# Kernel optimization log

Measured on AMD Instinct MI355X. Metric: run time of the kernel, lower is better.

Reference implementation:

```python
import jax, jax.numpy as jnp
import numpy as np

B, H, W = 32, 64, 1024
D, L, HEADS, E, TOPK, HID, V = 256, 6, 8, 8, 2, 1024, 8000


def _conv(x, w, b, s):
    y = jax.lax.conv_general_dilated(x, w, (s, s), [(1, 1), (1, 1)],
                                     dimension_numbers=('NCHW', 'OIHW', 'NCHW'))
    return y + b[None, :, None, None]


def _gelu(v):
    return jax.nn.gelu(v, approximate=False)


def _ln(x, g, b):
    m = x.mean(-1, keepdims=True)
    v = jnp.mean((x - m) ** 2, -1, keepdims=True)
    return (x - m) * jax.lax.rsqrt(v + 1e-5) * g + b


def _pos(t, c):
    pos = jnp.arange(t, dtype=jnp.float32)[:, None]
    div = jnp.exp(jnp.arange(0, c, 2, dtype=jnp.float32) * (-np.log(10000.0) / c))
    pe = jnp.zeros((t, c), jnp.float32)
    pe = pe.at[:, 0::2].set(jnp.sin(pos * div)).at[:, 1::2].set(jnp.cos(pos * div))
    return pe[None]


def _mha(y, w, b, ow, ob):
    Bq, T, Dm = y.shape
    hd = Dm // HEADS
    qkv = y @ w.T + b
    q, k, v = jnp.split(qkv, 3, axis=-1)
    sh = lambda z: z.reshape(Bq, T, HEADS, hd).transpose(0, 2, 1, 3)
    q, k, v = sh(q), sh(k), sh(v)
    att = jax.nn.softmax(jnp.einsum('bhqd,bhkd->bhqk', q, k) / np.sqrt(hd).astype(np.float32), axis=-1)
    o = jnp.einsum('bhqk,bhkd->bhqd', att, v).transpose(0, 2, 1, 3).reshape(Bq, T, Dm)
    return o @ ow.T + ob


def _moe(y, rw, rb, w1, b1, w2, b2):
    logits = y @ rw.T + rb                      # [B,T,E]
    tlog, tidx = jax.lax.top_k(logits, TOPK)
    gates = jax.nn.softmax(tlog, axis=-1)        # [B,T,K]
    # combine weights per expert: sum_k gate_k * 1[idx_k == e]
    comb = jnp.sum(gates[..., None] * jax.nn.one_hot(tidx, E, dtype=y.dtype), axis=-2)  # [B,T,E]
    h = _gelu(jnp.einsum('btd,ehd->beth', y, w1) + b1[None, :, None, :])
    eo = jnp.einsum('beth,edh->betd', h, w2) + b2[None, :, None, :]
    out = jnp.einsum('bte,betd->btd', comb, eo)
    imp = jax.nn.softmax(logits, axis=-1).mean(axis=(0, 1))
    aux = jnp.mean((imp - 1.0 / E) ** 2)
    return out, aux


def _forward(x, cw1, cb1, cw2, cb2, cw3, cb3, cw4, cb4,
             ln1_g, ln1_b, qkv_w, qkv_b, out_w, out_b,
             ln2_g, ln2_b, router_w, router_b, e_w1, e_b1, e_w2, e_b2,
             normf_g, normf_b, head_w, head_b):
    f = _gelu(_conv(x, cw1, cb1, 2))
    f = _gelu(_conv(f, cw2, cb2, 2))
    f = _gelu(_conv(f, cw3, cb3, 2))
    f = _gelu(_conv(f, cw4, cb4, 1))          # [B,D,H/8,W/8]
    tok = f.mean(axis=2).transpose(0, 2, 1)    # [B,T,D], T=W/8
    h = tok + _pos(tok.shape[1], tok.shape[2])
    aux_total = jnp.asarray(0.0, h.dtype)
    for l in range(L):
        y = _mha(_ln(h, ln1_g[l], ln1_b[l]), qkv_w[l], qkv_b[l], out_w[l], out_b[l])
        h = h + y
        y, aux = _moe(_ln(h, ln2_g[l], ln2_b[l]), router_w[l], router_b[l],
                      e_w1[l], e_b1[l], e_w2[l], e_b2[l])
        h = h + y
        aux_total = aux_total + aux
    h = _ln(h, normf_g, normf_b)
    logits = h @ head_w.T + head_b
    return logits, aux_total / L


def setup_inputs() -> dict:
    key = jax.random.key(0)
    ks = iter(jax.random.split(key, 40))
    nrm = lambda shape: jax.random.normal(next(ks), shape, jnp.float32) * 0.02
    d = {}
    d['x'] = jax.random.normal(next(ks), (B, 1, H, W), jnp.float32)
    d['cw1'] = nrm((D // 4, 1, 3, 3));      d['cb1'] = jnp.zeros((D // 4,), jnp.float32)
    d['cw2'] = nrm((D // 2, D // 4, 3, 3)); d['cb2'] = jnp.zeros((D // 2,), jnp.float32)
    d['cw3'] = nrm((D, D // 2, 3, 3));      d['cb3'] = jnp.zeros((D,), jnp.float32)
    d['cw4'] = nrm((D, D, 3, 3));           d['cb4'] = jnp.zeros((D,), jnp.float32)
    d['ln1_g'] = jnp.ones((L, D), jnp.float32); d['ln1_b'] = jnp.zeros((L, D), jnp.float32)
    d['qkv_w'] = nrm((L, 3 * D, D));        d['qkv_b'] = jnp.zeros((L, 3 * D), jnp.float32)
    d['out_w'] = nrm((L, D, D));            d['out_b'] = jnp.zeros((L, D), jnp.float32)
    d['ln2_g'] = jnp.ones((L, D), jnp.float32); d['ln2_b'] = jnp.zeros((L, D), jnp.float32)
    d['router_w'] = nrm((L, E, D));         d['router_b'] = jnp.zeros((L, E), jnp.float32)
    d['e_w1'] = nrm((L, E, HID, D));        d['e_b1'] = jnp.zeros((L, E, HID), jnp.float32)
    d['e_w2'] = nrm((L, E, D, HID));        d['e_b2'] = jnp.zeros((L, E, D), jnp.float32)
    d['normf_g'] = jnp.ones((D,), jnp.float32); d['normf_b'] = jnp.zeros((D,), jnp.float32)
    d['head_w'] = nrm((V, D));              d['head_b'] = jnp.zeros((V,), jnp.float32)
    return d


def reference(x, cw1, cb1, cw2, cb2, cw3, cb3, cw4, cb4,
              ln1_g, ln1_b, qkv_w, qkv_b, out_w, out_b,
              ln2_g, ln2_b, router_w, router_b, e_w1, e_b1, e_w2, e_b2,
              normf_g, normf_b, head_w, head_b):
    return _forward(x, cw1, cb1, cw2, cb2, cw3, cb3, cw4, cb4,
                    ln1_g, ln1_b, qkv_w, qkv_b, out_w, out_b,
                    ln2_g, ln2_b, router_w, router_b, e_w1, e_b1, e_w2, e_b2,
                    normf_g, normf_b, head_w, head_b)
```

## Files before the change

kernel.cpp:

```cpp
#include <hip/hip_runtime.h>
#include <math.h>


typedef __bf16 bf16x8 __attribute__((ext_vector_type(8)));
typedef float f32x4 __attribute__((ext_vector_type(4)));

__device__ __forceinline__ float gelu_f(float x) {
  return 0.5f * x * (1.0f + erff(x * 0.70710678118654752440f));
}

__global__ __launch_bounds__(256) void conv1_kernel(const float* __restrict__ x,
    const float* __restrict__ w, const float* __restrict__ bias, float* __restrict__ out) {
  int o = blockIdx.x * 256 + threadIdx.x;
  int co = o & 63, wo = (o >> 6) & 511, ho = (o >> 15) & 31, b = o >> 20;
  float acc = bias[co];
  const float* xp = x + (size_t)b * 65536;
  const float* wp = w + co * 9;
  #pragma unroll
  for (int kh = 0; kh < 3; kh++) {
    int hi = ho * 2 - 1 + kh;
    if ((unsigned)hi < 64u) {
      const float* row = xp + hi * 1024;
      #pragma unroll
      for (int kw = 0; kw < 3; kw++) {
        int wi = wo * 2 - 1 + kw;
        if ((unsigned)wi < 1024u) acc += row[wi] * wp[kh * 3 + kw];
      }
    }
  }
  out[o] = gelu_f(acc);
}

__global__ __launch_bounds__(256) void tr_cw_bf16_kernel(const float* __restrict__ w,
    __bf16* __restrict__ hi, __bf16* __restrict__ lo, int CI, int CO) {
  int i = blockIdx.x * 256 + threadIdx.x;
  if (i >= 9 * CI * CO) return;
  int ci = i % CI; int r = i / CI; int co = r % CO; int tap = r / CO;
  float x = w[(co * CI + ci) * 9 + tap];
  __bf16 h = (__bf16)x;
  __bf16 l = (__bf16)(x - (float)h);
  hi[i] = h; lo[i] = l;
}

template <int CI, int HI, int WI, int CO, int HO, int WO, int S>
__global__ __launch_bounds__(256) void convmfma_kernel(
    const float* __restrict__ in, const __bf16* __restrict__ wthi,
    const __bf16* __restrict__ wtlo, const float* __restrict__ bias,
    float* __restrict__ out) {
  __shared__ __bf16 Ah[128 * 40], Al[128 * 40], Bh[128 * 40], Bl[128 * 40];
  int tid = threadIdx.x;
  int lane = tid & 63, wid = tid >> 6;
  int wr = (wid >> 1) << 6, wc = (wid & 1) << 6;
  int lr = lane & 15;
  int lk = (lane >> 4) << 3;
  int tileN = blockIdx.x * 128, tileM = blockIdx.y * 128;
  int tr = tid >> 1;
  int tk = (tid & 1) << 4;
  int m = tileM + tr;
  int wo = m % WO, ho = (m / WO) % HO, b = m / (WO * HO);
  f32x4 acc[4][4];
  #pragma unroll
  for (int i = 0; i < 4; i++)
    #pragma unroll
    for (int j = 0; j < 4; j++) acc[i][j] = (f32x4){0.f, 0.f, 0.f, 0.f};

  for (int tap = 0; tap < 9; tap++) {
    int kh = tap / 3, kw = tap - kh * 3;
    int hi_ = ho * S - 1 + kh, wi_ = wo * S - 1 + kw;
    bool ok = ((unsigned)hi_ < (unsigned)HI) && ((unsigned)wi_ < (unsigned)WI);
    const float* ip = in + ((size_t)(b * HI + hi_) * WI + wi_) * CI + tk;
    const __bf16* wph = wthi + ((size_t)tap * CO + tileN + tr) * CI + tk;
    const __bf16* wpl = wtlo + ((size_t)tap * CO + tileN + tr) * CI + tk;
    for (int c0 = 0; c0 < CI; c0 += 32) {
      float v[16];
      #pragma unroll
      for (int q = 0; q < 4; q++) {
        float4 t4 = ok ? *(const float4*)(ip + c0 + q * 4) : (float4){0.f, 0.f, 0.f, 0.f};
        v[q * 4 + 0] = t4.x; v[q * 4 + 1] = t4.y; v[q * 4 + 2] = t4.z; v[q * 4 + 3] = t4.w;
      }
      bf16x8 hv0, hv1, lv0, lv1;
      #pragma unroll
      for (int j = 0; j < 8; j++) {
        __bf16 h0 = (__bf16)v[j];       hv0[j] = h0;
        lv0[j] = (__bf16)(v[j] - (float)h0);
        __bf16 h1 = (__bf16)v[8 + j];   hv1[j] = h1;
        lv1[j] = (__bf16)(v[8 + j] - (float)h1);
      }
      *(bf16x8*)&Ah[tr * 40 + tk] = hv0;
      *(bf16x8*)&Ah[tr * 40 + tk + 8] = hv1;
      *(bf16x8*)&Al[tr * 40 + tk] = lv0;
      *(bf16x8*)&Al[tr * 40 + tk + 8] = lv1;
      *(uint4*)&Bh[tr * 40 + tk] = *(const uint4*)(wph + c0);
      *(uint4*)&Bh[tr * 40 + tk + 8] = *(const uint4*)(wph + c0 + 8);
      *(uint4*)&Bl[tr * 40 + tk] = *(const uint4*)(wpl + c0);
      *(uint4*)&Bl[tr * 40 + tk + 8] = *(const uint4*)(wpl + c0 + 8);
      __syncthreads();
      bf16x8 ah[4], al[4];
      #pragma unroll
      for (int mt = 0; mt < 4; mt++) {
        int r = wr + mt * 16 + lr;
        ah[mt] = *(const bf16x8*)&Ah[r * 40 + lk];
        al[mt] = *(const bf16x8*)&Al[r * 40 + lk];
      }
      #pragma unroll
      for (int nt = 0; nt < 4; nt++) {
        int cc = wc + nt * 16 + lr;
        bf16x8 bh = *(const bf16x8*)&Bh[cc * 40 + lk];
        bf16x8 bl = *(const bf16x8*)&Bl[cc * 40 + lk];
        #pragma unroll
        for (int mt = 0; mt < 4; mt++) {
          acc[mt][nt] = __builtin_amdgcn_mfma_f32_16x16x32_bf16(ah[mt], bh, acc[mt][nt], 0, 0, 0);
          acc[mt][nt] = __builtin_amdgcn_mfma_f32_16x16x32_bf16(al[mt], bh, acc[mt][nt], 0, 0, 0);
          acc[mt][nt] = __builtin_amdgcn_mfma_f32_16x16x32_bf16(ah[mt], bl, acc[mt][nt], 0, 0, 0);
        }
      }
      __syncthreads();
    }
  }
  int drow = (lane >> 4) << 2;
  #pragma unroll
  for (int mt = 0; mt < 4; mt++) {
    #pragma unroll
    for (int nt = 0; nt < 4; nt++) {
      int orow = tileM + wr + mt * 16 + drow;
      int ocol = tileN + wc + nt * 16 + lr;
      float bv = bias[ocol];
      #pragma unroll
      for (int r = 0; r < 4; r++)
        out[(size_t)(orow + r) * CO + ocol] = gelu_f(acc[mt][nt][r] + bv);
    }
  }
}

__global__ __launch_bounds__(256) void gemm8_kernel(const float* __restrict__ A,
    const float* __restrict__ W, const float* __restrict__ bias, float* __restrict__ C,
    int N, int K, int addTo, int m0, int m1) {
  __shared__ float As[16][132];
  __shared__ float Ws[16][132];
  int tid = threadIdx.x;
  int tileN = blockIdx.x * 128, tileM = m0 + blockIdx.y * 128;
  int tx = tid & 15, ty = tid >> 4;
  int ar = tid >> 1, ak = (tid & 1) << 3;
  float acc[8][8];
  #pragma unroll
  for (int i = 0; i < 8; i++)
    #pragma unroll
    for (int j = 0; j < 8; j++) acc[i][j] = 0.0f;
  int arow = tileM + ar; if (arow > m1 - 1) arow = m1 - 1;
  int wrow = tileN + ar; if (wrow > N - 1) wrow = N - 1;
  const float* Ap = A + (size_t)arow * K + ak;
  const float* Wp = W + (size_t)wrow * K + ak;
  for (int k0 = 0; k0 < K; k0 += 16) {
    float4 a0 = *(const float4*)(Ap + k0);
    float4 a1 = *(const float4*)(Ap + k0 + 4);
    float4 w0 = *(const float4*)(Wp + k0);
    float4 w1 = *(const float4*)(Wp + k0 + 4);
    As[ak + 0][ar] = a0.x; As[ak + 1][ar] = a0.y; As[ak + 2][ar] = a0.z; As[ak + 3][ar] = a0.w;
    As[ak + 4][ar] = a1.x; As[ak + 5][ar] = a1.y; As[ak + 6][ar] = a1.z; As[ak + 7][ar] = a1.w;
    Ws[ak + 0][ar] = w0.x; Ws[ak + 1][ar] = w0.y; Ws[ak + 2][ar] = w0.z; Ws[ak + 3][ar] = w0.w;
    Ws[ak + 4][ar] = w1.x; Ws[ak + 5][ar] = w1.y; Ws[ak + 6][ar] = w1.z; Ws[ak + 7][ar] = w1.w;
    __syncthreads();
    #pragma unroll
    for (int kk = 0; kk < 16; kk++) {
      float4 av0 = *(const float4*)&As[kk][ty << 2];
      float4 av1 = *(const float4*)&As[kk][(ty << 2) + 64];
      float4 wv0 = *(const float4*)&Ws[kk][tx << 2];
      float4 wv1 = *(const float4*)&Ws[kk][(tx << 2) + 64];
      float a[8] = {av0.x, av0.y, av0.z, av0.w, av1.x, av1.y, av1.z, av1.w};
      float w[8] = {wv0.x, wv0.y, wv0.z, wv0.w, wv1.x, wv1.y, wv1.z, wv1.w};
      #pragma unroll
      for (int i = 0; i < 8; i++)
        #pragma unroll
        for (int j = 0; j < 8; j++) acc[i][j] += a[i] * w[j];
    }
    __syncthreads();
  }
  #pragma unroll
  for (int ih = 0; ih < 2; ih++) {
    #pragma unroll
    for (int i = 0; i < 4; i++) {
      int m = tileM + ih * 64 + (ty << 2) + i;
      if (m < m1) {
        float* Crow = C + (size_t)m * N;
        #pragma unroll
        for (int jh = 0; jh < 2; jh++) {
          #pragma unroll
          for (int j = 0; j < 4; j++) {
            int col = tileN + jh * 64 + (tx << 2) + j;
            if (col < N) {
              float v = acc[ih * 4 + i][jh * 4 + j] + bias[col];
              if (addTo) Crow[col] += v; else Crow[col] = v;
            }
          }
        }
      }
    }
  }
}

__global__ __launch_bounds__(256) void token_kernel(const float* __restrict__ f, float* __restrict__ h) {
  int i = blockIdx.x * 256 + threadIdx.x;
  int d = i & 255, t = (i >> 8) & 127, b = i >> 15;
  const float* fp = f + ((size_t)(b * 8) * 128 + t) * 256 + d;
  float s = 0.0f;
  #pragma unroll
  for (int ho = 0; ho < 8; ho++) s += fp[(size_t)ho * 32768];
  float tok = s * 0.125f;
  int i2 = d & ~1;
  float freq = expf(-(float)i2 * (float)(9.210340371976184 / 256.0));
  float ang = (float)t * freq;
  float pe = (d & 1) ? cosf(ang) : sinf(ang);
  h[i] = tok + pe;
}

__global__ __launch_bounds__(64) void ln_kernel(const float* __restrict__ in, float* __restrict__ out,
    const float* __restrict__ g, const float* __restrict__ b) {
  int row = blockIdx.x;
  int lane = threadIdx.x;
  float4 v = ((const float4*)(in + (size_t)row * 256))[lane];
  float s = v.x + v.y + v.z + v.w;
  float s2 = v.x * v.x + v.y * v.y + v.z * v.z + v.w * v.w;
  #pragma unroll
  for (int m = 1; m < 64; m <<= 1) { s += __shfl_xor(s, m); s2 += __shfl_xor(s2, m); }
  float mean = s * (1.0f / 256.0f);
  float var = s2 * (1.0f / 256.0f) - mean * mean;
  float rstd = rsqrtf(var + 1e-5f);
  float4 gv = ((const float4*)g)[lane];
  float4 bv = ((const float4*)b)[lane];
  float4 ov;
  ov.x = (v.x - mean) * rstd * gv.x + bv.x;
  ov.y = (v.y - mean) * rstd * gv.y + bv.y;
  ov.z = (v.z - mean) * rstd * gv.z + bv.z;
  ov.w = (v.w - mean) * rstd * gv.w + bv.w;
  ((float4*)(out + (size_t)row * 256))[lane] = ov;
}

__global__ __launch_bounds__(256) void gemm128_kernel(const float* __restrict__ A, const float* __restrict__ W,
    const float* __restrict__ bias, float* __restrict__ C, int N, int K, int addTo, int m0, int m1) {
  __shared__ float As[16][136];
  __shared__ float Ws[16][68];
  int tid = threadIdx.x;
  int tileN = blockIdx.x * 64, tileM = m0 + blockIdx.y * 128;
  int ar = tid >> 1, ak = (tid & 1) << 3;
  int wr = tid >> 2, wk = (tid & 3) << 2;
  int tx = tid & 15, ty = tid >> 4;
  float acc[8][4];
  #pragma unroll
  for (int i = 0; i < 8; i++)
    #pragma unroll
    for (int j = 0; j < 4; j++) acc[i][j] = 0.0f;
  int arow = tileM + ar; if (arow > m1 - 1) arow = m1 - 1;
  const float* Ap = A + (size_t)arow * K + ak;
  const float* Wp = W + (size_t)(tileN + wr) * K + wk;
  for (int k0 = 0; k0 < K; k0 += 16) {
    float4 a0 = *(const float4*)(Ap + k0);
    float4 a1 = *(const float4*)(Ap + k0 + 4);
    float4 w4 = *(const float4*)(Wp + k0);
    As[ak + 0][ar] = a0.x; As[ak + 1][ar] = a0.y; As[ak + 2][ar] = a0.z; As[ak + 3][ar] = a0.w;
    As[ak + 4][ar] = a1.x; As[ak + 5][ar] = a1.y; As[ak + 6][ar] = a1.z; As[ak + 7][ar] = a1.w;
    Ws[wk + 0][wr] = w4.x; Ws[wk + 1][wr] = w4.y; Ws[wk + 2][wr] = w4.z; Ws[wk + 3][wr] = w4.w;
    __syncthreads();
    #pragma unroll
    for (int kk = 0; kk < 16; kk++) {
      float4 av0 = *(const float4*)&As[kk][ty << 3];
      float4 av1 = *(const float4*)&As[kk][(ty << 3) + 4];
      float4 wv = *(const float4*)&Ws[kk][tx << 2];
      float a[8] = {av0.x, av0.y, av0.z, av0.w, av1.x, av1.y, av1.z, av1.w};
      float w[4] = {wv.x, wv.y, wv.z, wv.w};
      #pragma unroll
      for (int i = 0; i < 8; i++)
        #pragma unroll
        for (int j = 0; j < 4; j++) acc[i][j] += a[i] * w[j];
    }
    __syncthreads();
  }
  #pragma unroll
  for (int i = 0; i < 8; i++) {
    int m = tileM + (ty << 3) + i;
    if (m < m1) {
      float* Crow = C + (size_t)m * N + tileN + (tx << 2);
      #pragma unroll
      for (int j = 0; j < 4; j++) {
        float v = acc[i][j] + bias[tileN + (tx << 2) + j];
        if (addTo) Crow[j] += v; else Crow[j] = v;
      }
    }
  }
}

__global__ __launch_bounds__(256) void gemm_kernel(const float* __restrict__ A, const float* __restrict__ W,
    const float* __restrict__ bias, float* __restrict__ C, int N, int K, int addTo, int m0, int m1) {
  __shared__ float As[16][68];
  __shared__ float Ws[16][68];
  int tid = threadIdx.x;
  int tileN = blockIdx.x * 64, tileM = m0 + blockIdx.y * 64;
  int lr = tid >> 2, lk = (tid & 3) << 2;
  int tx = tid & 15, ty = tid >> 4;
  float acc[4][4];
  #pragma unroll
  for (int i = 0; i < 4; i++)
    #pragma unroll
    for (int j = 0; j < 4; j++) acc[i][j] = 0.0f;
  int arow = tileM + lr; if (arow > m1 - 1) arow = m1 - 1;
  const float* Ap = A + (size_t)arow * K + lk;
  const float* Wp = W + (size_t)(tileN + lr) * K + lk;
  for (int k0 = 0; k0 < K; k0 += 16) {
    float4 a4 = *(const float4*)(Ap + k0);
    float4 w4 = *(const float4*)(Wp + k0);
    As[lk + 0][lr] = a4.x; As[lk + 1][lr] = a4.y; As[lk + 2][lr] = a4.z; As[lk + 3][lr] = a4.w;
    Ws[lk + 0][lr] = w4.x; Ws[lk + 1][lr] = w4.y; Ws[lk + 2][lr] = w4.z; Ws[lk + 3][lr] = w4.w;
    __syncthreads();
    #pragma unroll
    for (int kk = 0; kk < 16; kk++) {
      float4 av = *(const float4*)&As[kk][ty << 2];
      float4 wv = *(const float4*)&Ws[kk][tx << 2];
      float a[4] = {av.x, av.y, av.z, av.w};
      float w[4] = {wv.x, wv.y, wv.z, wv.w};
      #pragma unroll
      for (int i = 0; i < 4; i++)
        #pragma unroll
        for (int j = 0; j < 4; j++) acc[i][j] += a[i] * w[j];
    }
    __syncthreads();
  }
  #pragma unroll
  for (int i = 0; i < 4; i++) {
    int m = tileM + (ty << 2) + i;
    if (m < m1) {
      float* Crow = C + (size_t)m * N + tileN + (tx << 2);
      #pragma unroll
      for (int j = 0; j < 4; j++) {
        float v = acc[i][j] + bias[tileN + (tx << 2) + j];
        if (addTo) Crow[j] += v; else Crow[j] = v;
      }
    }
  }
}

__global__ __launch_bounds__(256) void head_row0_kernel(const float* __restrict__ y,
    const float* __restrict__ W, const float* __restrict__ bias, float* __restrict__ out) {
  __shared__ float yrow[256];
  int tid = threadIdx.x;
  yrow[tid] = y[tid];
  __syncthreads();
  for (int col = tid; col < 8000; col += 256) {
    const float4* wp = (const float4*)(W + (size_t)col * 256);
    float acc = 0.0f;
    for (int d = 0; d < 64; d++) {
      float4 w4 = wp[d];
      acc += w4.x * yrow[d * 4] + w4.y * yrow[d * 4 + 1] + w4.z * yrow[d * 4 + 2] + w4.w * yrow[d * 4 + 3];
    }
    out[col] = acc + bias[col];
  }
}

__global__ __launch_bounds__(128) void attn_kernel(const float* __restrict__ qkv, float* __restrict__ o) {
  __shared__ float Ks[128][33];
  __shared__ float Vs[128][33];
  int b = blockIdx.x >> 3, hh = blockIdx.x & 7;
  int t = threadIdx.x;
  const float* base = qkv + (size_t)(b * 128 + t) * 768 + hh * 32;
  float q[32];
  #pragma unroll
  for (int i = 0; i < 32; i += 4) {
    float4 v4 = *(const float4*)(base + i);
    q[i] = v4.x; q[i + 1] = v4.y; q[i + 2] = v4.z; q[i + 3] = v4.w;
    float4 k4 = *(const float4*)(base + 256 + i);
    Ks[t][i] = k4.x; Ks[t][i + 1] = k4.y; Ks[t][i + 2] = k4.z; Ks[t][i + 3] = k4.w;
    float4 w4 = *(const float4*)(base + 512 + i);
    Vs[t][i] = w4.x; Vs[t][i + 1] = w4.y; Vs[t][i + 2] = w4.z; Vs[t][i + 3] = w4.w;
  }
  __syncthreads();
  const float scale = 0.17677669529663687f;
  float m = -1e30f;
  for (int j = 0; j < 128; j++) {
    float s = 0.0f;
    #pragma unroll
    for (int i = 0; i < 32; i++) s += q[i] * Ks[j][i];
    m = fmaxf(m, s);
  }
  m *= scale;
  float l = 0.0f;
  float acc[32];
  #pragma unroll
  for (int i = 0; i < 32; i++) acc[i] = 0.0f;
  for (int j = 0; j < 128; j++) {
    float s = 0.0f;
    #pragma unroll
    for (int i = 0; i < 32; i++) s += q[i] * Ks[j][i];
    float p = __expf(s * scale - m);
    l += p;
    #pragma unroll
    for (int i = 0; i < 32; i++) acc[i] += p * Vs[j][i];
  }
  float inv = 1.0f / l;
  float* op = o + (size_t)(b * 128 + t) * 256 + hh * 32;
  #pragma unroll
  for (int i = 0; i < 32; i++) op[i] = acc[i] * inv;
}

__global__ __launch_bounds__(256) void router_kernel(const float* __restrict__ y,
    const float* __restrict__ rw, const float* __restrict__ rb,
    int* __restrict__ eidx, float* __restrict__ egate, float* __restrict__ imp) {
  int token = blockIdx.x * 256 + threadIdx.x;
  const float4* yp4 = (const float4*)(y + (size_t)token * 256);
  float logit[8];
  #pragma unroll
  for (int e = 0; e < 8; e++) {
    const float4* wp = (const float4*)(rw + e * 256);
    float acc = 0.0f;
    for (int d = 0; d < 64; d++) {
      float4 w4 = wp[d]; float4 v4 = yp4[d];
      acc += w4.x * v4.x + w4.y * v4.y + w4.z * v4.z + w4.w * v4.w;
    }
    logit[e] = acc + rb[e];
  }
  float mx = logit[0];
  #pragma unroll
  for (int e = 1; e < 8; e++) mx = fmaxf(mx, logit[e]);
  float p[8]; float sum = 0.0f;
  #pragma unroll
  for (int e = 0; e < 8; e++) { p[e] = __expf(logit[e] - mx); sum += p[e]; }
  float inv = 1.0f / sum;
  #pragma unroll
  for (int e = 0; e < 8; e++) {
    float pe = p[e] * inv;
    #pragma unroll
    for (int msk = 1; msk < 64; msk <<= 1) pe += __shfl_xor(pe, msk);
    if ((threadIdx.x & 63) == 0) atomicAdd(&imp[e], pe);
  }
  float m0 = -1e30f, m1 = -1e30f; int i0 = 0, i1 = 0;
  #pragma unroll
  for (int e = 0; e < 8; e++) {
    if (logit[e] > m0) { m1 = m0; i1 = i0; m0 = logit[e]; i0 = e; }
    else if (logit[e] > m1) { m1 = logit[e]; i1 = e; }
  }
  float g1 = __expf(m1 - m0);
  float g0 = 1.0f / (1.0f + g1);
  g1 *= g0;
  eidx[token * 2] = i0; eidx[token * 2 + 1] = i1;
  egate[token * 2] = g0; egate[token * 2 + 1] = g1;
}

__global__ __launch_bounds__(256) void tr_w1_kernel(const float* __restrict__ w, float4* __restrict__ o) {
  int i = blockIdx.x * 256 + threadIdx.x;
  int r = i & 1023, d4 = (i >> 10) & 63, e = i >> 16;
  o[i] = *(const float4*)(w + ((size_t)(e * 1024 + r)) * 256 + (d4 << 2));
}
__global__ __launch_bounds__(256) void tr_w2_kernel(const float* __restrict__ w, float4* __restrict__ o) {
  int i = blockIdx.x * 256 + threadIdx.x;
  int dd = i & 255, j4 = (i >> 8) & 255, e = i >> 16;
  o[i] = *(const float4*)(w + ((size_t)(e * 256 + dd)) * 1024 + (j4 << 2));
}

__global__ __launch_bounds__(256) void moe_kernel(const float* __restrict__ y,
    const float4* __restrict__ w1t, const float* __restrict__ b1,
    const float4* __restrict__ w2t, const float* __restrict__ b2,
    const int* __restrict__ eidx, const float* __restrict__ egate,
    float* __restrict__ h) {
  __shared__ float4 ylds[16][64];
  __shared__ __align__(16) float hlds[16][512];
  __shared__ int list[128];
  __shared__ int cnt;
  int tid = threadIdx.x;
  int e = blockIdx.x >> 7;
  int c = (blockIdx.x >> 1) & 63;
  int jc = blockIdx.x & 1;
  if (tid == 0) cnt = 0;
  __syncthreads();
  if (tid < 128) {
    int s = c * 128 + tid;
    if (eidx[s] == e) list[atomicAdd(&cnt, 1)] = s;
  }
  __syncthreads();
  int n = cnt;
  if (n == 0) return;
  int g8 = tid >> 7;
  int dd = tid & 127;
  const float4* w1p = w1t + (size_t)e * 65536 + jc * 512 + tid;
  const float4* w2p = w2t + (size_t)e * 65536 + dd;
  float bb0 = b1[e * 1024 + jc * 512 + tid];
  float bb1 = b1[e * 1024 + jc * 512 + 256 + tid];
  float b2v0 = jc ? 0.0f : b2[e * 256 + dd];
  float b2v1 = jc ? 0.0f : b2[e * 256 + dd + 128];
  const float4* y4 = (const float4*)y;
  for (int base = 0; base < n; base += 16) {
    int nt = (n - base) < 16 ? (n - base) : 16;
    for (int idx = tid; idx < 16 * 64; idx += 256) {
      int ti = idx >> 6, d4 = idx & 63;
      int slot = list[base + (ti < nt ? ti : 0)];
      ylds[ti][d4] = y4[(size_t)(slot >> 1) * 64 + d4];
    }
    __syncthreads();
    float h0[16], h1[16];
    #pragma unroll
    for (int i = 0; i < 16; i++) { h0[i] = bb0; h1[i] = bb1; }
    for (int d4 = 0; d4 < 64; d4++) {
      float4 wa = w1p[(size_t)d4 * 1024];
      float4 wb = w1p[(size_t)d4 * 1024 + 256];
      #pragma unroll
      for (int i = 0; i < 16; i++) {
        float4 yv = ylds[i][d4];
        h0[i] += wa.x * yv.x + wa.y * yv.y + wa.z * yv.z + wa.w * yv.w;
        h1[i] += wb.x * yv.x + wb.y * yv.y + wb.z * yv.z + wb.w * yv.w;
      }
    }
    #pragma unroll
    for (int i = 0; i < 16; i++) {
      hlds[i][tid] = gelu_f(h0[i]);
      hlds[i][256 + tid] = gelu_f(h1[i]);
    }
    __syncthreads();
    float acc2a[8], acc2b[8];
    #pragma unroll
    for (int i = 0; i < 8; i++) { acc2a[i] = 0.0f; acc2b[i] = 0.0f; }
    for (int j4 = 0; j4 < 128; j4++) {
      float4 wa = w2p[(size_t)(jc * 128 + j4) * 256];
      float4 wb = w2p[(size_t)(jc * 128 + j4) * 256 + 128];
      #pragma unroll
      for (int i = 0; i < 8; i++) {
        float4 hv = *(const float4*)&hlds[g8 * 8 + i][j4 * 4];
        acc2a[i] += wa.x * hv.x + wa.y * hv.y + wa.z * hv.z + wa.w * hv.w;
        acc2b[i] += wb.x * hv.x + wb.y * hv.y + wb.z * hv.z + wb.w * hv.w;
      }
    }
    __syncthreads();
    #pragma unroll
    for (int i = 0; i < 8; i++) {
      int ii = g8 * 8 + i;
      if (ii < nt) {
        int slot = list[base + ii];
        float g = egate[slot];
        float* hp = h + (size_t)(slot >> 1) * 256;
        atomicAdd(hp + dd, g * (acc2a[i] + b2v0));
        atomicAdd(hp + dd + 128, g * (acc2b[i] + b2v1));
      }
    }
  }
}

__global__ void zero_kernel(float* __restrict__ p, int n) {
  int i = blockIdx.x * blockDim.x + threadIdx.x;
  if (i < n) p[i] = 0.0f;
}

__global__ void aux_kernel(const float* __restrict__ imp, float* __restrict__ out) {
  float total = 0.0f;
  for (int l = 0; l < 6; l++) {
    float a = 0.0f;
    for (int e = 0; e < 8; e++) {
      float v = imp[l * 8 + e] * (1.0f / 4096.0f) - 0.125f;
      a += v * v;
    }
    total += a * 0.125f;
  }
  out[0] = total * (1.0f / 6.0f);
}

extern "C" void kernel_launch(void* const* d_in, const int* in_sizes, int n_in,
                              void* d_out, int out_size, void* d_ws, size_t ws_size,
                              hipStream_t stream) {
  const float* x      = (const float*)d_in[0];
  const float* cw1    = (const float*)d_in[1];
  const float* cb1    = (const float*)d_in[2];
  const float* cw2    = (const float*)d_in[3];
  const float* cb2    = (const float*)d_in[4];
  const float* cw3    = (const float*)d_in[5];
  const float* cb3    = (const float*)d_in[6];
  const float* cw4    = (const float*)d_in[7];
  const float* cb4    = (const float*)d_in[8];
  const float* ln1_g  = (const float*)d_in[9];
  const float* ln1_b  = (const float*)d_in[10];
  const float* qkv_w  = (const float*)d_in[11];
  const float* qkv_b  = (const float*)d_in[12];
  const float* out_w  = (const float*)d_in[13];
  const float* out_b  = (const float*)d_in[14];
  const float* ln2_g  = (const float*)d_in[15];
  const float* ln2_b  = (const float*)d_in[16];
  const float* router_w = (const float*)d_in[17];
  const float* router_b = (const float*)d_in[18];
  const float* e_w1   = (const float*)d_in[19];
  const float* e_b1   = (const float*)d_in[20];
  const float* e_w2   = (const float*)d_in[21];
  const float* e_b2   = (const float*)d_in[22];
  const float* normf_g = (const float*)d_in[23];
  const float* normf_b = (const float*)d_in[24];
  const float* head_w = (const float*)d_in[25];
  const float* head_b = (const float*)d_in[26];
  float* out = (float*)d_out;
  (void)d_ws; (void)ws_size;

  float* y = out;
  float* h = out + 1048576;
  float* S = out + 2097152;
  float* c2 = S;
  float* c1 = S + 16777216;
  float* c3 = S + 16777216;
  float* c4 = S;
  __bf16* cw2h = (__bf16*)(S + 25165824);
  __bf16* cw2l = (__bf16*)(S + 25202688);
  __bf16* cw3h = (__bf16*)(S + 25239552);
  __bf16* cw3l = (__bf16*)(S + 25387008);
  __bf16* cw4h = (__bf16*)(S + 25534464);
  __bf16* cw4l = (__bf16*)(S + 25829376);
  float* qkvb = S;
  float* ob   = S + 3145728;
  float* y2   = S + 4194304;
  int*   eidx  = (int*)(S + 5242880);
  float* egate = S + 5242880 + 8192;
  float* imp   = S + 5242880 + 16384;
  float* w1t   = S + 5767168;
  float* w2t   = S + 7864320;

  tr_cw_bf16_kernel<<<(9 * 64 * 128 + 255) / 256, 256, 0, stream>>>(cw2, cw2h, cw2l, 64, 128);
  tr_cw_bf16_kernel<<<(9 * 128 * 256 + 255) / 256, 256, 0, stream>>>(cw3, cw3h, cw3l, 128, 256);
  tr_cw_bf16_kernel<<<(9 * 256 * 256 + 255) / 256, 256, 0, stream>>>(cw4, cw4h, cw4l, 256, 256);

  for (int c = 0; c < 4; c++) {
    const float* xc = x + (size_t)c * 8 * 65536;
    conv1_kernel<<<32768, 256, 0, stream>>>(xc, cw1, cb1, c1);
    convmfma_kernel<64, 32, 512, 128, 16, 256, 2>
        <<<dim3(1, 256), 256, 0, stream>>>(c1, cw2h, cw2l, cb2, c2 + (size_t)c * 4194304);
  }
  convmfma_kernel<128, 16, 256, 256, 8, 128, 2>
      <<<dim3(2, 256), 256, 0, stream>>>(c2, cw3h, cw3l, cb3, c3);
  convmfma_kernel<256, 8, 128, 256, 8, 128, 1>
      <<<dim3(2, 256), 256, 0, stream>>>(c3, cw4h, cw4l, cb4, c4);
  token_kernel<<<4096, 256, 0, stream>>>(c4, h);
  zero_kernel<<<1, 64, 0, stream>>>(imp, 48);

  for (int l = 0; l < 6; l++) {
    tr_w1_kernel<<<2048, 256, 0, stream>>>(e_w1 + (size_t)l * 8 * 1024 * 256, (float4*)w1t);
    tr_w2_kernel<<<2048, 256, 0, stream>>>(e_w2 + (size_t)l * 8 * 256 * 1024, (float4*)w2t);
    ln_kernel<<<4096, 64, 0, stream>>>(h, y, ln1_g + l * 256, ln1_b + l * 256);
    gemm128_kernel<<<dim3(12, 32), 256, 0, stream>>>(y, qkv_w + (size_t)l * 768 * 256, qkv_b + l * 768,
                                                     qkvb, 768, 256, 0, 0, 4096);
    attn_kernel<<<256, 128, 0, stream>>>(qkvb, ob);
    gemm128_kernel<<<dim3(4, 32), 256, 0, stream>>>(ob, out_w + (size_t)l * 256 * 256, out_b + l * 256,
                                                    h, 256, 256, 1, 0, 4096);
    ln_kernel<<<4096, 64, 0, stream>>>(h, y2, ln2_g + l * 256, ln2_b + l * 256);
    router_kernel<<<16, 256, 0, stream>>>(y2, router_w + l * 8 * 256, router_b + l * 8,
                                          eidx, egate, imp + l * 8);
    moe_kernel<<<1024, 256, 0, stream>>>(y2, (const float4*)w1t, e_b1 + l * 8 * 1024,
                                         (const float4*)w2t, e_b2 + l * 8 * 256,
                                         eidx, egate, h);
  }

  ln_kernel<<<4096, 64, 0, stream>>>(h, y, normf_g, normf_b);
  aux_kernel<<<1, 1, 0, stream>>>(imp, out + 32768000);

  gemm8_kernel<<<dim3(63, 31), 256, 0, stream>>>(y, head_w, head_b, out, 8000, 256, 0, 132, 4096);
  gemm8_kernel<<<dim3(63, 1), 256, 0, stream>>>(y, head_w, head_b, out, 8000, 256, 0, 5, 132);
  gemm_kernel<<<dim3(125, 1), 256, 0, stream>>>(y, head_w, head_b, out, 8000, 256, 0, 1, 5);
  head_row0_kernel<<<1, 256, 0, stream>>>(y, head_w, head_b, out);
}
```

Baseline: 4.589 ms.

## Run MoE expert FFN on bf16 MFMA with hi/lo split-precision weights

Replaces the scalar fp32 FMA MoE expert kernel with a matrix-core version. Weights are split into bf16 high and low parts, and each GEMM uses three MFMAs (hi*hi, lo*hi, hi*lo) to approach fp32 accuracy. The per-layer weight transpose kernels become a simple elementwise split kernel. B operands are read straight from global memory without LDS staging, so the kernel may end up memory-bound, and the three-pass split triples the MFMA count.

```diff
diff --git a/kernel.cpp b/kernel.cpp
--- a/kernel.cpp
+++ b/kernel.cpp
@@ -40,6 +40,15 @@
   __bf16 h = (__bf16)x;
   __bf16 l = (__bf16)(x - (float)h);
   hi[i] = h; lo[i] = l;
+}
+
+__global__ __launch_bounds__(256) void split_bf16_kernel(const float* __restrict__ w,
+    __bf16* __restrict__ hi, __bf16* __restrict__ lo, int nelem) {
+  int i = blockIdx.x * 256 + threadIdx.x;
+  if (i >= nelem) return;
+  float x = w[i];
+  __bf16 h = (__bf16)x;
+  hi[i] = h; lo[i] = (__bf16)(x - (float)h);
 }
 
 template <int CI, int HI, int WI, int CO, int HO, int WO, int S>
@@ -442,27 +451,22 @@
   egate[token * 2] = g0; egate[token * 2 + 1] = g1;
 }
 
-__global__ __launch_bounds__(256) void tr_w1_kernel(const float* __restrict__ w, float4* __restrict__ o) {
-  int i = blockIdx.x * 256 + threadIdx.x;
-  int r = i & 1023, d4 = (i >> 10) & 63, e = i >> 16;
-  o[i] = *(const float4*)(w + ((size_t)(e * 1024 + r)) * 256 + (d4 << 2));
-}
-__global__ __launch_bounds__(256) void tr_w2_kernel(const float* __restrict__ w, float4* __restrict__ o) {
-  int i = blockIdx.x * 256 + threadIdx.x;
-  int dd = i & 255, j4 = (i >> 8) & 255, e = i >> 16;
-  o[i] = *(const float4*)(w + ((size_t)(e * 256 + dd)) * 1024 + (j4 << 2));
-}
-
-__global__ __launch_bounds__(256) void moe_kernel(const float* __restrict__ y,
-    const float4* __restrict__ w1t, const float* __restrict__ b1,
-    const float4* __restrict__ w2t, const float* __restrict__ b2,
+__global__ __launch_bounds__(256) void moe_mfma_kernel(const float* __restrict__ y,
+    const __bf16* __restrict__ w1h, const __bf16* __restrict__ w1l,
+    const float* __restrict__ b1,
+    const __bf16* __restrict__ w2h, const __bf16* __restrict__ w2l,
+    const float* __restrict__ b2,
     const int* __restrict__ eidx, const float* __restrict__ egate,
     float* __restrict__ h) {
-  __shared__ float4 ylds[16][64];
-  __shared__ __align__(16) float hlds[16][512];
+  __shared__ __bf16 Ah[16 * 264], Al[16 * 264];
+  __shared__ __bf16 Hh[16 * 520], Hl[16 * 520];
   __shared__ int list[128];
   __shared__ int cnt;
   int tid = threadIdx.x;
+  int lane = tid & 63, wid = tid >> 6;
+  int lr = lane & 15;
+  int lk = (lane >> 4) << 3;
+  int drow = (lane >> 4) << 2;
   int e = blockIdx.x >> 7;
   int c = (blockIdx.x >> 1) & 63;
   int jc = blockIdx.x & 1;
@@ -475,67 +479,111 @@
   __syncthreads();
   int n = cnt;
   if (n == 0) return;
-  int g8 = tid >> 7;
-  int dd = tid & 127;
-  const float4* w1p = w1t + (size_t)e * 65536 + jc * 512 + tid;
-  const float4* w2p = w2t + (size_t)e * 65536 + dd;
-  float bb0 = b1[e * 1024 + jc * 512 + tid];
-  float bb1 = b1[e * 1024 + jc * 512 + 256 + tid];
-  float b2v0 = jc ? 0.0f : b2[e * 256 + dd];
-  float b2v1 = jc ? 0.0f : b2[e * 256 + dd + 128];
-  const float4* y4 = (const float4*)y;
+  const __bf16* w1he = w1h + ((size_t)e * 1024 + jc * 512) * 256;
+  const __bf16* w1le = w1l + ((size_t)e * 1024 + jc * 512) * 256;
+  const __bf16* w2he = w2h + (size_t)e * 256 * 1024 + jc * 512;
+  const __bf16* w2le = w2l + (size_t)e * 256 * 1024 + jc * 512;
+  const float* b1e = b1 + e * 1024 + jc * 512;
+  const float* b2e = b2 + e * 256;
+  int sr = tid >> 4;
+  int sk = (tid & 15) << 4;
   for (int base = 0; base < n; base += 16) {
     int nt = (n - base) < 16 ? (n - base) : 16;
-    for (int idx = tid; idx < 16 * 64; idx += 256) {
-      int ti = idx >> 6, d4 = idx & 63;
-      int slot = list[base + (ti < nt ? ti : 0)];
-      ylds[ti][d4] = y4[(size_t)(slot >> 1) * 64 + d4];
-    }
-    __syncthreads();
-    float h0[16], h1[16];
-    #pragma unroll
-    for (int i = 0; i < 16; i++) { h0[i] = bb0; h1[i] = bb1; }
-    for (int d4 = 0; d4 < 64; d4++) {
-      float4 wa = w1p[(size_t)d4 * 1024];
-      float4 wb = w1p[(size_t)d4 * 1024 + 256];
-      #pragma unroll
-      for (int i = 0; i < 16; i++) {
-        float4 yv = ylds[i][d4];
-        h0[i] += wa.x * yv.x + wa.y * yv.y + wa.z * yv.z + wa.w * yv.w;
-        h1[i] += wb.x * yv.x + wb.y * yv.y + wb.z * yv.z + wb.w * yv.w;
-      }
-    }
-    #pragma unroll
-    for (int i = 0; i < 16; i++) {
-      hlds[i][tid] = gelu_f(h0[i]);
-      hlds[i][256 + tid] = gelu_f(h1[i]);
-    }
-    __syncthreads();
-    float acc2a[8], acc2b[8];
-    #pragma unroll
-    for (int i = 0; i < 8; i++) { acc2a[i] = 0.0f; acc2b[i] = 0.0f; }
-    for (int j4 = 0; j4 < 128; j4++) {
-      float4 wa = w2p[(size_t)(jc * 128 + j4) * 256];
-      float4 wb = w2p[(size_t)(jc * 128 + j4) * 256 + 128];
-      #pragma unroll
-      for (int i = 0; i < 8; i++) {
-        float4 hv = *(const float4*)&hlds[g8 * 8 + i][j4 * 4];
-        acc2a[i] += wa.x * hv.x + wa.y * hv.y + wa.z * hv.z + wa.w * hv.w;
-        acc2b[i] += wb.x * hv.x + wb.y * hv.y + wb.z * hv.z + wb.w * hv.w;
-      }
-    }
-    __syncthreads();
-    #pragma unroll
-    for (int i = 0; i < 8; i++) {
-      int ii = g8 * 8 + i;
-      if (ii < nt) {
-        int slot = list[base + ii];
-        float g = egate[slot];
-        float* hp = h + (size_t)(slot >> 1) * 256;
-        atomicAdd(hp + dd, g * (acc2a[i] + b2v0));
-        atomicAdd(hp + dd + 128, g * (acc2b[i] + b2v1));
-      }
-    }
+    {
+      int ti = sr < nt ? sr : 0;
+      int slot = list[base + ti];
+      const float* yp = y + (size_t)(slot >> 1) * 256 + sk;
+      float v[16];
+      #pragma unroll
+      for (int q = 0; q < 4; q++) {
+        float4 t4 = *(const float4*)(yp + q * 4);
+        v[q * 4 + 0] = t4.x; v[q * 4 + 1] = t4.y; v[q * 4 + 2] = t4.z; v[q * 4 + 3] = t4.w;
+      }
+      bf16x8 hv0, hv1, lv0, lv1;
+      #pragma unroll
+      for (int j = 0; j < 8; j++) {
+        __bf16 h0 = (__bf16)v[j];     hv0[j] = h0;
+        lv0[j] = (__bf16)(v[j] - (float)h0);
+        __bf16 h1 = (__bf16)v[8 + j]; hv1[j] = h1;
+        lv1[j] = (__bf16)(v[8 + j] - (float)h1);
+      }
+      *(bf16x8*)&Ah[sr * 264 + sk] = hv0;
+      *(bf16x8*)&Ah[sr * 264 + sk + 8] = hv1;
+      *(bf16x8*)&Al[sr * 264 + sk] = lv0;
+      *(bf16x8*)&Al[sr * 264 + sk + 8] = lv1;
+    }
+    __syncthreads();
+    {
+      f32x4 acc[8];
+      #pragma unroll
+      for (int ct = 0; ct < 8; ct++) acc[ct] = (f32x4){0.f, 0.f, 0.f, 0.f};
+      #pragma unroll
+      for (int ks = 0; ks < 8; ks++) {
+        bf16x8 ah = *(const bf16x8*)&Ah[lr * 264 + lk + ks * 32];
+        bf16x8 al = *(const bf16x8*)&Al[lr * 264 + lk + ks * 32];
+        #pragma unroll
+        for (int ct = 0; ct < 8; ct++) {
+          int col = wid * 128 + ct * 16 + lr;
+          const __bf16* bph = w1he + (size_t)col * 256 + lk + ks * 32;
+          const __bf16* bpl = w1le + (size_t)col * 256 + lk + ks * 32;
+          bf16x8 bh = *(const bf16x8*)bph;
+          bf16x8 bl = *(const bf16x8*)bpl;
+          acc[ct] = __builtin_amdgcn_mfma_f32_16x16x32_bf16(ah, bh, acc[ct], 0, 0, 0);
+          acc[ct] = __builtin_amdgcn_mfma_f32_16x16x32_bf16(al, bh, acc[ct], 0, 0, 0);
+          acc[ct] = __builtin_amdgcn_mfma_f32_16x16x32_bf16(ah, bl, acc[ct], 0, 0, 0);
+        }
+      }
+      #pragma unroll
+      for (int ct = 0; ct < 8; ct++) {
+        int col = wid * 128 + ct * 16 + lr;
+        float bb = b1e[col];
+        #pragma unroll
+        for (int r = 0; r < 4; r++) {
+          float hv = gelu_f(acc[ct][r] + bb);
+          __bf16 hh = (__bf16)hv;
+          int trow = drow + r;
+          Hh[trow * 520 + col] = hh;
+          Hl[trow * 520 + col] = (__bf16)(hv - (float)hh);
+        }
+      }
+    }
+    __syncthreads();
+    {
+      f32x4 acc2[4];
+      #pragma unroll
+      for (int ct = 0; ct < 4; ct++) acc2[ct] = (f32x4){0.f, 0.f, 0.f, 0.f};
+      #pragma unroll
+      for (int ks = 0; ks < 16; ks++) {
+        bf16x8 ahh = *(const bf16x8*)&Hh[lr * 520 + lk + ks * 32];
+        bf16x8 ahl = *(const bf16x8*)&Hl[lr * 520 + lk + ks * 32];
+        #pragma unroll
+        for (int ct = 0; ct < 4; ct++) {
+          int d = wid * 64 + ct * 16 + lr;
+          const __bf16* bph = w2he + (size_t)d * 1024 + lk + ks * 32;
+          const __bf16* bpl = w2le + (size_t)d * 1024 + lk + ks * 32;
+          bf16x8 bh = *(const bf16x8*)bph;
+          bf16x8 bl = *(const bf16x8*)bpl;
+          acc2[ct] = __builtin_amdgcn_mfma_f32_16x16x32_bf16(ahh, bh, acc2[ct], 0, 0, 0);
+          acc2[ct] = __builtin_amdgcn_mfma_f32_16x16x32_bf16(ahl, bh, acc2[ct], 0, 0, 0);
+          acc2[ct] = __builtin_amdgcn_mfma_f32_16x16x32_bf16(ahh, bl, acc2[ct], 0, 0, 0);
+        }
+      }
+      #pragma unroll
+      for (int ct = 0; ct < 4; ct++) {
+        int d = wid * 64 + ct * 16 + lr;
+        float b2v = jc ? 0.0f : b2e[d];
+        #pragma unroll
+        for (int r = 0; r < 4; r++) {
+          int trow = drow + r;
+          if (trow < nt) {
+            int slot = list[base + trow];
+            float g = egate[slot];
+            atomicAdd(h + (size_t)(slot >> 1) * 256 + d, g * (acc2[ct][r] + b2v));
+          }
+        }
+      }
+    }
+    __syncthreads();
   }
 }
 
@@ -611,6 +659,10 @@
   float* imp   = S + 5242880 + 16384;
   float* w1t   = S + 5767168;
   float* w2t   = S + 7864320;
+  __bf16* w1hp = (__bf16*)w1t;
+  __bf16* w1lp = (__bf16*)(w1t + 1048576);
+  __bf16* w2hp = (__bf16*)w2t;
+  __bf16* w2lp = (__bf16*)(w2t + 1048576);
 
   tr_cw_bf16_kernel<<<(9 * 64 * 128 + 255) / 256, 256, 0, stream>>>(cw2, cw2h, cw2l, 64, 128);
   tr_cw_bf16_kernel<<<(9 * 128 * 256 + 255) / 256, 256, 0, stream>>>(cw3, cw3h, cw3l, 128, 256);
@@ -630,8 +682,8 @@
   zero_kernel<<<1, 64, 0, stream>>>(imp, 48);
 
   for (int l = 0; l < 6; l++) {
-    tr_w1_kernel<<<2048, 256, 0, stream>>>(e_w1 + (size_t)l * 8 * 1024 * 256, (float4*)w1t);
-    tr_w2_kernel<<<2048, 256, 0, stream>>>(e_w2 + (size_t)l * 8 * 256 * 1024, (float4*)w2t);
+    split_bf16_kernel<<<8192, 256, 0, stream>>>(e_w1 + (size_t)l * 2097152, w1hp, w1lp, 2097152);
+    split_bf16_kernel<<<8192, 256, 0, stream>>>(e_w2 + (size_t)l * 2097152, w2hp, w2lp, 2097152);
     ln_kernel<<<4096, 64, 0, stream>>>(h, y, ln1_g + l * 256, ln1_b + l * 256);
     gemm128_kernel<<<dim3(12, 32), 256, 0, stream>>>(y, qkv_w + (size_t)l * 768 * 256, qkv_b + l * 768,
                                                      qkvb, 768, 256, 0, 0, 4096);
@@ -641,9 +693,9 @@
     ln_kernel<<<4096, 64, 0, stream>>>(h, y2, ln2_g + l * 256, ln2_b + l * 256);
     router_kernel<<<16, 256, 0, stream>>>(y2, router_w + l * 8 * 256, router_b + l * 8,
                                           eidx, egate, imp + l * 8);
-    moe_kernel<<<1024, 256, 0, stream>>>(y2, (const float4*)w1t, e_b1 + l * 8 * 1024,
-                                         (const float4*)w2t, e_b2 + l * 8 * 256,
-                                         eidx, egate, h);
+    moe_mfma_kernel<<<1024, 256, 0, stream>>>(y2, w1hp, w1lp, e_b1 + l * 8 * 1024,
+                                              w2hp, w2lp, e_b2 + l * 8 * 256,
+                                              eidx, egate, h);
   }
 
   ln_kernel<<<4096, 64, 0, stream>>>(h, y, normf_g, normf_b);
```

Measured after the change: 6.199 ms. 1.35x slower.
